# Performance work log

Measured on AMD Instinct MI355X. Metric: run time of the kernel, lower is better.

## Reference

```python
import jax, jax.numpy as jnp
import numpy as np

B, T, IN, H, FC, OUT = 512, 1024, 64, 128, 128, 1


def _glorot(key, shape, fan):
    bound = 1.0 / np.sqrt(fan)
    return jax.random.uniform(key, shape, jnp.float32, -bound, bound)


def setup_inputs() -> dict:
    key = jax.random.key(0)
    ks = jax.random.split(key, 16)
    inp = {"x": jax.random.normal(ks[0], (B, T, IN), jnp.float32)}
    # GRU layer 0 (input IN -> H), layer 1 (H -> H). PyTorch layout: [3H, in], [3H, H]
    inp["W_ih0"] = _glorot(ks[1], (3 * H, IN), H)
    inp["W_hh0"] = _glorot(ks[2], (3 * H, H), H)
    inp["b_ih0"] = _glorot(ks[3], (3 * H,), H)
    inp["b_hh0"] = _glorot(ks[4], (3 * H,), H)
    inp["W_ih1"] = _glorot(ks[5], (3 * H, H), H)
    inp["W_hh1"] = _glorot(ks[6], (3 * H, H), H)
    inp["b_ih1"] = _glorot(ks[7], (3 * H,), H)
    inp["b_hh1"] = _glorot(ks[8], (3 * H,), H)
    inp["fc1_w"] = _glorot(ks[9], (FC, H), H)
    inp["fc1_b"] = _glorot(ks[10], (FC,), H)
    inp["fc2_w"] = _glorot(ks[11], (OUT, FC), FC)
    inp["fc2_b"] = _glorot(ks[12], (OUT,), FC)
    return inp


def _gru_layer(x_seq, W_ih, W_hh, b_ih, b_hh):
    # x_seq: [T, B, in]. Precompute all input projections in one big GEMM.
    xg = jnp.einsum("tbi,gi->tbg", x_seq, W_ih) + b_ih  # [T, B, 3H]
    h0 = jnp.zeros((x_seq.shape[1], W_hh.shape[1]), x_seq.dtype)

    def step(h, xg_t):
        hg = h @ W_hh.T + b_hh  # [B, 3H]
        xr, xz, xn = jnp.split(xg_t, 3, axis=-1)
        hr, hz, hn = jnp.split(hg, 3, axis=-1)
        r = jax.nn.sigmoid(xr + hr)
        z = jax.nn.sigmoid(xz + hz)
        n = jnp.tanh(xn + r * hn)
        h_new = (1.0 - z) * n + z * h
        return h_new, h_new

    _, hs = jax.lax.scan(step, h0, xg)
    return hs  # [T, B, H]


def reference(x, W_ih0, W_hh0, b_ih0, b_hh0, W_ih1, W_hh1, b_ih1, b_hh1,
              fc1_w, fc1_b, fc2_w, fc2_b):
    xs = jnp.transpose(x, (1, 0, 2))  # [T, B, IN]
    h1 = _gru_layer(xs, W_ih0, W_hh0, b_ih0, b_hh0)  # dropout inactive (eval)
    h2 = _gru_layer(h1, W_ih1, W_hh1, b_ih1, b_hh1)
    last = h2[-1]  # [B, H] == gru_out[:, -1, :]
    y = jax.nn.relu(last @ fc1_w.T + fc1_b)
    return y @ fc2_w.T + fc2_b  # [B, OUT]
```

## Files before the change

### kernel.cpp

```cpp
#include <hip/hip_runtime.h>
#include <hip/hip_fp16.h>
#include <stdint.h>

#define TT   1024
#define NIN  64
#define HH   128
#define RPB  16
#define NWG  32
#define NTHR 512

#define FB_IH0 0
#define FB_HH0 48
#define FB_IH1 144
#define FB_HH1 240

typedef _Float16 f16x8 __attribute__((ext_vector_type(8)));
typedef float    f32x4 __attribute__((ext_vector_type(4)));
typedef _Float16 half2v __attribute__((ext_vector_type(2)));

__device__ __forceinline__ uint32_t pack2f(float a, float b) {
    half2v v; v[0] = (_Float16)a; v[1] = (_Float16)b;
    return __builtin_bit_cast(uint32_t, v);
}
__device__ __forceinline__ f16x8 bc8(uint4 u) { return __builtin_bit_cast(f16x8, u); }
__device__ __forceinline__ float sigm(float v)     { return 1.f / (1.f + __expf(-v)); }
__device__ __forceinline__ float tanhfast(float v) { return 2.f / (1.f + __expf(-2.f * v)) - 1.f; }

#define MF(c_, a_, b_) c_ = __builtin_amdgcn_mfma_f32_16x16x32_f16(bc8(a_), bc8(b_), c_, 0, 0, 0);

#define UNPK2(a_, b_, s_) { half2v t_ = __builtin_bit_cast(half2v, s_); a_ = (float)t_[0]; b_ = (float)t_[1]; }

#define CMB(ri_, CR_, CZ_, CX_, CH_, BR_, BZ_, BXX_, BHH_, HO_, NH_) { \
    float rg_ = sigm(CR_[ri_] + BR_);                                   \
    float zg_ = sigm(CZ_[ri_] + BZ_);                                   \
    float ng_ = tanhfast(CX_[ri_] + BXX_ + rg_ * (CH_[ri_] + BHH_));    \
    NH_ = ng_ + zg_ * (HO_ - ng_); HO_ = NH_; }

#define BARS() { asm volatile("s_waitcnt lgkmcnt(0)" ::: "memory");  \
                 __builtin_amdgcn_s_barrier();                        \
                 __builtin_amdgcn_sched_barrier(0);                   \
                 asm volatile("" ::: "memory"); }

__global__ __launch_bounds__(256) void pack_frags(
    const float* __restrict__ Wih0, const float* __restrict__ Whh0,
    const float* __restrict__ Wih1, const float* __restrict__ Whh1,
    uint4* __restrict__ ws)
{
    const int tid = blockIdx.x * 256 + threadIdx.x;
    const int f = tid >> 6, l = tid & 63;
    const float* W; int K, mt, kt;
    if (f < 48)       { W = Wih0; K = NIN; mt = f >> 1;        kt = f & 1; }
    else if (f < 144) { W = Whh0; K = HH;  mt = (f - 48) >> 2;  kt = (f - 48) & 3; }
    else if (f < 240) { W = Wih1; K = HH;  mt = (f - 144) >> 2; kt = (f - 144) & 3; }
    else              { W = Whh1; K = HH;  mt = (f - 240) >> 2; kt = (f - 240) & 3; }
    const float* s = W + (mt * 16 + (l & 15)) * K + kt * 32 + (l >> 4) * 8;
    uint4 o;
    o.x = pack2f(s[0], s[1]); o.y = pack2f(s[2], s[3]);
    o.z = pack2f(s[4], s[5]); o.w = pack2f(s[6], s[7]);
    ws[tid] = o;
}

__global__ __launch_bounds__(NTHR)
__attribute__((amdgpu_waves_per_eu(2, 2)))
void gru_mfma(
    const float* __restrict__ x, const uint4* __restrict__ wsA,
    const float* __restrict__ bih0, const float* __restrict__ bhh0,
    const float* __restrict__ bih1, const float* __restrict__ bhh1,
    const float* __restrict__ fc1w, const float* __restrict__ fc1b,
    const float* __restrict__ fc2w, const float* __restrict__ fc2b,
    float* __restrict__ out)
{
    __shared__ uint4 xF[2][2][64];
    __shared__ uint4 h0F[2][4][64];
    __shared__ uint4 h1F[2][4][64];
    __shared__ float h1f[RPB][HH];
    __shared__ float pFC[RPB][HH];
    __shared__ float p2[RPB][8];

    const int lid = threadIdx.x, w = lid >> 6, l = lid & 63;
    const int row0 = blockIdx.x * RPB;

#define DECLF(nm, idx) uint4 nm = wsA[(idx) * 64 + l];
    DECLF(a0r_i0, FB_IH0 + (w)*2 + 0)     DECLF(a0r_i1, FB_IH0 + (w)*2 + 1)
    DECLF(a0r_h0, FB_HH0 + (w)*4 + 0)     DECLF(a0r_h1, FB_HH0 + (w)*4 + 1)
    DECLF(a0r_h2, FB_HH0 + (w)*4 + 2)     DECLF(a0r_h3, FB_HH0 + (w)*4 + 3)
    DECLF(a0z_i0, FB_IH0 + (w+8)*2 + 0)   DECLF(a0z_i1, FB_IH0 + (w+8)*2 + 1)
    DECLF(a0z_h0, FB_HH0 + (w+8)*4 + 0)   DECLF(a0z_h1, FB_HH0 + (w+8)*4 + 1)
    DECLF(a0z_h2, FB_HH0 + (w+8)*4 + 2)   DECLF(a0z_h3, FB_HH0 + (w+8)*4 + 3)
    DECLF(a0n_i0, FB_IH0 + (16+w)*2 + 0)  DECLF(a0n_i1, FB_IH0 + (16+w)*2 + 1)
    DECLF(a0n_h0, FB_HH0 + (16+w)*4 + 0)  DECLF(a0n_h1, FB_HH0 + (16+w)*4 + 1)
    DECLF(a0n_h2, FB_HH0 + (16+w)*4 + 2)  DECLF(a0n_h3, FB_HH0 + (16+w)*4 + 3)
    DECLF(a1r_i0, FB_IH1 + (w)*4 + 0)     DECLF(a1r_i1, FB_IH1 + (w)*4 + 1)
    DECLF(a1r_i2, FB_IH1 + (w)*4 + 2)     DECLF(a1r_i3, FB_IH1 + (w)*4 + 3)
    DECLF(a1r_h0, FB_HH1 + (w)*4 + 0)     DECLF(a1r_h1, FB_HH1 + (w)*4 + 1)
    DECLF(a1r_h2, FB_HH1 + (w)*4 + 2)     DECLF(a1r_h3, FB_HH1 + (w)*4 + 3)
    DECLF(a1z_i0, FB_IH1 + (w+8)*4 + 0)   DECLF(a1z_i1, FB_IH1 + (w+8)*4 + 1)
    DECLF(a1z_i2, FB_IH1 + (w+8)*4 + 2)   DECLF(a1z_i3, FB_IH1 + (w+8)*4 + 3)
    DECLF(a1z_h0, FB_HH1 + (w+8)*4 + 0)   DECLF(a1z_h1, FB_HH1 + (w+8)*4 + 1)
    DECLF(a1z_h2, FB_HH1 + (w+8)*4 + 2)   DECLF(a1z_h3, FB_HH1 + (w+8)*4 + 3)
    DECLF(a1n_i0, FB_IH1 + (16+w)*4 + 0)  DECLF(a1n_i1, FB_IH1 + (16+w)*4 + 1)
    DECLF(a1n_i2, FB_IH1 + (16+w)*4 + 2)  DECLF(a1n_i3, FB_IH1 + (16+w)*4 + 3)
    DECLF(a1n_h0, FB_HH1 + (16+w)*4 + 0)  DECLF(a1n_h1, FB_HH1 + (16+w)*4 + 1)
    DECLF(a1n_h2, FB_HH1 + (16+w)*4 + 2)  DECLF(a1n_h3, FB_HH1 + (16+w)*4 + 3)

    const int j0 = 16 * w + 4 * (l >> 4);
    uint32_t B0r01 = pack2f(bih0[j0]+bhh0[j0],       bih0[j0+1]+bhh0[j0+1]);
    uint32_t B0r23 = pack2f(bih0[j0+2]+bhh0[j0+2],   bih0[j0+3]+bhh0[j0+3]);
    uint32_t B0z01 = pack2f(bih0[128+j0]+bhh0[128+j0],     bih0[129+j0]+bhh0[129+j0]);
    uint32_t B0z23 = pack2f(bih0[130+j0]+bhh0[130+j0],     bih0[131+j0]+bhh0[131+j0]);
    uint32_t B0x01 = pack2f(bih0[256+j0], bih0[257+j0]);
    uint32_t B0x23 = pack2f(bih0[258+j0], bih0[259+j0]);
    uint32_t B0h01 = pack2f(bhh0[256+j0], bhh0[257+j0]);
    uint32_t B0h23 = pack2f(bhh0[258+j0], bhh0[259+j0]);
    uint32_t B1r01 = pack2f(bih1[j0]+bhh1[j0],       bih1[j0+1]+bhh1[j0+1]);
    uint32_t B1r23 = pack2f(bih1[j0+2]+bhh1[j0+2],   bih1[j0+3]+bhh1[j0+3]);
    uint32_t B1z01 = pack2f(bih1[128+j0]+bhh1[128+j0],     bih1[129+j0]+bhh1[129+j0]);
    uint32_t B1z23 = pack2f(bih1[130+j0]+bhh1[130+j0],     bih1[131+j0]+bhh1[131+j0]);
    uint32_t B1x01 = pack2f(bih1[256+j0], bih1[257+j0]);
    uint32_t B1x23 = pack2f(bih1[258+j0], bih1[259+j0]);
    uint32_t B1h01 = pack2f(bhh1[256+j0], bhh1[257+j0]);
    uint32_t B1h23 = pack2f(bhh1[258+j0], bhh1[259+j0]);

    float h0o0 = 0.f, h0o1 = 0.f, h0o2 = 0.f, h0o3 = 0.f;
    float h1o0 = 0.f, h1o1 = 0.f, h1o2 = 0.f, h1o3 = 0.f;

    { uint4 z4 = {0u,0u,0u,0u};
      (&h0F[0][0][0])[lid] = z4;
      (&h1F[0][0][0])[lid] = z4; }

    const int xrow = lid >> 5, xk = (lid & 31) * 2;
    const float* xbase = x + (size_t)(row0 + xrow) * TT * NIN + xk;
    const int xoff = ((xk >> 5) << 10) + (((((xk & 31) >> 3) * 16) + xrow) << 4) + ((xk & 7) << 1);
    float2 xr2;
    { float2 v0 = *(const float2*)xbase;
      *(uint32_t*)((char*)&xF[0][0][0] + xoff) = pack2f(v0.x, v0.y);
      xr2 = *(const float2*)(xbase + NIN); }

    const int hoff = ((w >> 1) << 10)
                   + ((((2 * (w & 1) + ((l >> 4) >> 1)) * 16) + (l & 15)) << 4)
                   + (((l >> 4) & 1) << 3);

    __syncthreads();

    for (int i = 0; i <= TT; ++i) {
        const int p = i & 1;
        const uint4* bb0 = &h0F[p][0][0];
        uint4 bh00 = bb0[l], bh01 = bb0[64+l], bh02 = bb0[128+l], bh03 = bb0[192+l];

        if (i < TT) {
            const uint4* bxv = &xF[p][0][0];
            uint4 bx0 = bxv[l], bx1 = bxv[64 + l];
            f32x4 cr = {0,0,0,0}, cz = {0,0,0,0}, cx = {0,0,0,0}, ch = {0,0,0,0};
            MF(cr, a0r_i0, bx0)  MF(cr, a0r_i1, bx1)
            MF(cr, a0r_h0, bh00) MF(cr, a0r_h1, bh01) MF(cr, a0r_h2, bh02) MF(cr, a0r_h3, bh03)
            MF(cz, a0z_i0, bx0)  MF(cz, a0z_i1, bx1)
            MF(cz, a0z_h0, bh00) MF(cz, a0z_h1, bh01) MF(cz, a0z_h2, bh02) MF(cz, a0z_h3, bh03)
            MF(cx, a0n_i0, bx0)  MF(cx, a0n_i1, bx1)
            MF(ch, a0n_h0, bh00) MF(ch, a0n_h1, bh01) MF(ch, a0n_h2, bh02) MF(ch, a0n_h3, bh03)
            float vr0,vr1,vr2,vr3, vz0,vz1,vz2,vz3, vx0,vx1,vx2,vx3, vh0,vh1,vh2,vh3;
            UNPK2(vr0,vr1,B0r01) UNPK2(vr2,vr3,B0r23)
            UNPK2(vz0,vz1,B0z01) UNPK2(vz2,vz3,B0z23)
            UNPK2(vx0,vx1,B0x01) UNPK2(vx2,vx3,B0x23)
            UNPK2(vh0,vh1,B0h01) UNPK2(vh2,vh3,B0h23)
            float nh0, nh1, nh2, nh3;
            CMB(0, cr,cz,cx,ch, vr0,vz0,vx0,vh0, h0o0, nh0)
            CMB(1, cr,cz,cx,ch, vr1,vz1,vx1,vh1, h0o1, nh1)
            CMB(2, cr,cz,cx,ch, vr2,vz2,vx2,vh2, h0o2, nh2)
            CMB(3, cr,cz,cx,ch, vr3,vz3,vx3,vh3, h0o3, nh3)
            uint2 hw; hw.x = pack2f(nh0, nh1); hw.y = pack2f(nh2, nh3);
            *(uint2*)((char*)&h0F[1 - p][0][0] + hoff) = hw;
        }

        if (i >= 1) {
            const uint4* bb1 = &h1F[p][0][0];
            uint4 bh10 = bb1[l], bh11 = bb1[64+l], bh12 = bb1[128+l], bh13 = bb1[192+l];
            f32x4 cr = {0,0,0,0}, cz = {0,0,0,0}, cx = {0,0,0,0}, ch = {0,0,0,0};
            MF(cr, a1r_i0, bh00) MF(cr, a1r_i1, bh01) MF(cr, a1r_i2, bh02) MF(cr, a1r_i3, bh03)
            MF(cr, a1r_h0, bh10) MF(cr, a1r_h1, bh11) MF(cr, a1r_h2, bh12) MF(cr, a1r_h3, bh13)
            MF(cz, a1z_i0, bh00) MF(cz, a1z_i1, bh01) MF(cz, a1z_i2, bh02) MF(cz, a1z_i3, bh03)
            MF(cz, a1z_h0, bh10) MF(cz, a1z_h1, bh11) MF(cz, a1z_h2, bh12) MF(cz, a1z_h3, bh13)
            MF(cx, a1n_i0, bh00) MF(cx, a1n_i1, bh01) MF(cx, a1n_i2, bh02) MF(cx, a1n_i3, bh03)
            MF(ch, a1n_h0, bh10) MF(ch, a1n_h1, bh11) MF(ch, a1n_h2, bh12) MF(ch, a1n_h3, bh13)
            float vr0,vr1,vr2,vr3, vz0,vz1,vz2,vz3, vx0,vx1,vx2,vx3, vh0,vh1,vh2,vh3;
            UNPK2(vr0,vr1,B1r01) UNPK2(vr2,vr3,B1r23)
            UNPK2(vz0,vz1,B1z01) UNPK2(vz2,vz3,B1z23)
            UNPK2(vx0,vx1,B1x01) UNPK2(vx2,vx3,B1x23)
            UNPK2(vh0,vh1,B1h01) UNPK2(vh2,vh3,B1h23)
            float nh0, nh1, nh2, nh3;
            CMB(0, cr,cz,cx,ch, vr0,vz0,vx0,vh0, h1o0, nh0)
            CMB(1, cr,cz,cx,ch, vr1,vz1,vx1,vh1, h1o1, nh1)
            CMB(2, cr,cz,cx,ch, vr2,vz2,vx2,vh2, h1o2, nh2)
            CMB(3, cr,cz,cx,ch, vr3,vz3,vx3,vh3, h1o3, nh3)
            uint2 hw; hw.x = pack2f(nh0, nh1); hw.y = pack2f(nh2, nh3);
            *(uint2*)((char*)&h1F[1 - p][0][0] + hoff) = hw;
        }

        if (i + 1 < TT)
            *(uint32_t*)((char*)&xF[1 - p][0][0] + xoff) = pack2f(xr2.x, xr2.y);
        if (i + 2 < TT)
            xr2 = *(const float2*)(xbase + (size_t)(i + 2) * NIN);

        BARS();
    }

    { f32x4 hv; hv[0] = h1o0; hv[1] = h1o1; hv[2] = h1o2; hv[3] = h1o3;
      *(f32x4*)&h1f[l & 15][16 * w + 4 * (l >> 4)] = hv; }
    __syncthreads();

    { const int fcj = lid & 127, rb = lid >> 7;
      float a0 = fc1b[fcj], a1 = a0, a2 = a0, a3 = a0;
      const float* fw = fc1w + fcj * HH;
      #pragma unroll 4
      for (int k = 0; k < HH; ++k) {
          float wv = fw[k];
          a0 = fmaf(wv, h1f[rb][k], a0);
          a1 = fmaf(wv, h1f[rb + 4][k], a1);
          a2 = fmaf(wv, h1f[rb + 8][k], a2);
          a3 = fmaf(wv, h1f[rb + 12][k], a3);
      }
      float s2 = fc2w[fcj];
      pFC[rb][fcj]      = fmaxf(a0, 0.f) * s2;
      pFC[rb + 4][fcj]  = fmaxf(a1, 0.f) * s2;
      pFC[rb + 8][fcj]  = fmaxf(a2, 0.f) * s2;
      pFC[rb + 12][fcj] = fmaxf(a3, 0.f) * s2; }
    __syncthreads();
    if (lid < 128) {
        const int r = lid >> 3, seg = lid & 7;
        float s = 0.f;
        #pragma unroll
        for (int m2 = 0; m2 < 16; ++m2) s += pFC[r][seg * 16 + m2];
        p2[r][seg] = s;
    }
    __syncthreads();
    if (lid < RPB) {
        float s = fc2b[0];
        #pragma unroll
        for (int q = 0; q < 8; ++q) s += p2[lid][q];
        out[row0 + lid] = s;
    }
}

extern "C" void kernel_launch(void* const* d_in, const int* in_sizes, int n_in,
                              void* d_out, int out_size, void* d_ws, size_t ws_size,
                              hipStream_t stream) {
    const float* x    = (const float*)d_in[0];
    const float* Wih0 = (const float*)d_in[1];
    const float* Whh0 = (const float*)d_in[2];
    const float* bih0 = (const float*)d_in[3];
    const float* bhh0 = (const float*)d_in[4];
    const float* Wih1 = (const float*)d_in[5];
    const float* Whh1 = (const float*)d_in[6];
    const float* bih1 = (const float*)d_in[7];
    const float* bhh1 = (const float*)d_in[8];
    const float* fc1w = (const float*)d_in[9];
    const float* fc1b = (const float*)d_in[10];
    const float* fc2w = (const float*)d_in[11];
    const float* fc2b = (const float*)d_in[12];

    uint4* ws = (uint4*)d_ws;

    pack_frags<<<dim3(84), dim3(256), 0, stream>>>(Wih0, Whh0, Wih1, Whh1, ws);
    gru_mfma<<<dim3(NWG), dim3(NTHR), 0, stream>>>(
        x, ws, bih0, bhh0, bih1, bhh1, fc1w, fc1b, fc2w, fc2b, (float*)d_out);
}
```

Before: 2.228 ms.

## Fold biases into MFMA accumulator init and keep fp32 hidden state in LDS

```diff
diff --git a/kernel.cpp b/kernel.cpp
--- a/kernel.cpp
+++ b/kernel.cpp
@@ -30,11 +30,11 @@
 
 #define UNPK2(a_, b_, s_) { half2v t_ = __builtin_bit_cast(half2v, s_); a_ = (float)t_[0]; b_ = (float)t_[1]; }
 
-#define CMB(ri_, CR_, CZ_, CX_, CH_, BR_, BZ_, BXX_, BHH_, HO_, NH_) { \
-    float rg_ = sigm(CR_[ri_] + BR_);                                   \
-    float zg_ = sigm(CZ_[ri_] + BZ_);                                   \
-    float ng_ = tanhfast(CX_[ri_] + BXX_ + rg_ * (CH_[ri_] + BHH_));    \
-    NH_ = ng_ + zg_ * (HO_ - ng_); HO_ = NH_; }
+#define CMB2(ri_, HOv_, NH_) { \
+    float rg_ = sigm(cr[ri_]); \
+    float zg_ = sigm(cz[ri_]); \
+    float ng_ = tanhfast(fmaf(rg_, ch[ri_], cx[ri_])); \
+    NH_ = ng_ + zg_ * (HOv_[ri_] - ng_); }
 
 #define BARS() { asm volatile("s_waitcnt lgkmcnt(0)" ::: "memory");  \
                  __builtin_amdgcn_s_barrier();                        \
@@ -73,6 +73,7 @@
     __shared__ uint4 xF[2][2][64];
     __shared__ uint4 h0F[2][4][64];
     __shared__ uint4 h1F[2][4][64];
+    __shared__ f32x4 holdF[2][NTHR];
     __shared__ float h1f[RPB][HH];
     __shared__ float pFC[RPB][HH];
     __shared__ float p2[RPB][8];
@@ -121,12 +122,11 @@
     uint32_t B1h01 = pack2f(bhh1[256+j0], bhh1[257+j0]);
     uint32_t B1h23 = pack2f(bhh1[258+j0], bhh1[259+j0]);
 
-    float h0o0 = 0.f, h0o1 = 0.f, h0o2 = 0.f, h0o3 = 0.f;
-    float h1o0 = 0.f, h1o1 = 0.f, h1o2 = 0.f, h1o3 = 0.f;
-
     { uint4 z4 = {0u,0u,0u,0u};
       (&h0F[0][0][0])[lid] = z4;
-      (&h1F[0][0][0])[lid] = z4; }
+      (&h1F[0][0][0])[lid] = z4;
+      f32x4 zf = {0.f,0.f,0.f,0.f};
+      holdF[0][lid] = zf; holdF[1][lid] = zf; }
 
     const int xrow = lid >> 5, xk = (lid & 31) * 2;
     const float* xbase = x + (size_t)(row0 + xrow) * TT * NIN + xk;
@@ -146,51 +146,51 @@
         const int p = i & 1;
         const uint4* bb0 = &h0F[p][0][0];
         uint4 bh00 = bb0[l], bh01 = bb0[64+l], bh02 = bb0[128+l], bh03 = bb0[192+l];
+        const uint4* bb1 = &h1F[p][0][0];
+        uint4 bh10 = bb1[l], bh11 = bb1[64+l], bh12 = bb1[128+l], bh13 = bb1[192+l];
 
         if (i < TT) {
             const uint4* bxv = &xF[p][0][0];
             uint4 bx0 = bxv[l], bx1 = bxv[64 + l];
-            f32x4 cr = {0,0,0,0}, cz = {0,0,0,0}, cx = {0,0,0,0}, ch = {0,0,0,0};
+            float u0,u1,u2,u3;
+            UNPK2(u0,u1,B0r01) UNPK2(u2,u3,B0r23)  f32x4 cr = {u0,u1,u2,u3};
+            UNPK2(u0,u1,B0z01) UNPK2(u2,u3,B0z23)  f32x4 cz = {u0,u1,u2,u3};
+            UNPK2(u0,u1,B0x01) UNPK2(u2,u3,B0x23)  f32x4 cx = {u0,u1,u2,u3};
+            UNPK2(u0,u1,B0h01) UNPK2(u2,u3,B0h23)  f32x4 ch = {u0,u1,u2,u3};
             MF(cr, a0r_i0, bx0)  MF(cr, a0r_i1, bx1)
             MF(cr, a0r_h0, bh00) MF(cr, a0r_h1, bh01) MF(cr, a0r_h2, bh02) MF(cr, a0r_h3, bh03)
             MF(cz, a0z_i0, bx0)  MF(cz, a0z_i1, bx1)
             MF(cz, a0z_h0, bh00) MF(cz, a0z_h1, bh01) MF(cz, a0z_h2, bh02) MF(cz, a0z_h3, bh03)
             MF(cx, a0n_i0, bx0)  MF(cx, a0n_i1, bx1)
             MF(ch, a0n_h0, bh00) MF(ch, a0n_h1, bh01) MF(ch, a0n_h2, bh02) MF(ch, a0n_h3, bh03)
-            float vr0,vr1,vr2,vr3, vz0,vz1,vz2,vz3, vx0,vx1,vx2,vx3, vh0,vh1,vh2,vh3;
-            UNPK2(vr0,vr1,B0r01) UNPK2(vr2,vr3,B0r23)
-            UNPK2(vz0,vz1,B0z01) UNPK2(vz2,vz3,B0z23)
-            UNPK2(vx0,vx1,B0x01) UNPK2(vx2,vx3,B0x23)
-            UNPK2(vh0,vh1,B0h01) UNPK2(vh2,vh3,B0h23)
+            f32x4 hold = holdF[0][lid];
             float nh0, nh1, nh2, nh3;
-            CMB(0, cr,cz,cx,ch, vr0,vz0,vx0,vh0, h0o0, nh0)
-            CMB(1, cr,cz,cx,ch, vr1,vz1,vx1,vh1, h0o1, nh1)
-            CMB(2, cr,cz,cx,ch, vr2,vz2,vx2,vh2, h0o2, nh2)
-            CMB(3, cr,cz,cx,ch, vr3,vz3,vx3,vh3, h0o3, nh3)
+            CMB2(0, hold, nh0) CMB2(1, hold, nh1) CMB2(2, hold, nh2) CMB2(3, hold, nh3)
+            f32x4 hn_; hn_[0]=nh0; hn_[1]=nh1; hn_[2]=nh2; hn_[3]=nh3;
+            holdF[0][lid] = hn_;
             uint2 hw; hw.x = pack2f(nh0, nh1); hw.y = pack2f(nh2, nh3);
             *(uint2*)((char*)&h0F[1 - p][0][0] + hoff) = hw;
         }
 
+        __builtin_amdgcn_sched_barrier(0);
+
         if (i >= 1) {
-            const uint4* bb1 = &h1F[p][0][0];
-            uint4 bh10 = bb1[l], bh11 = bb1[64+l], bh12 = bb1[128+l], bh13 = bb1[192+l];
-            f32x4 cr = {0,0,0,0}, cz = {0,0,0,0}, cx = {0,0,0,0}, ch = {0,0,0,0};
+            float u0,u1,u2,u3;
+            UNPK2(u0,u1,B1r01) UNPK2(u2,u3,B1r23)  f32x4 cr = {u0,u1,u2,u3};
+            UNPK2(u0,u1,B1z01) UNPK2(u2,u3,B1z23)  f32x4 cz = {u0,u1,u2,u3};
+            UNPK2(u0,u1,B1x01) UNPK2(u2,u3,B1x23)  f32x4 cx = {u0,u1,u2,u3};
+            UNPK2(u0,u1,B1h01) UNPK2(u2,u3,B1h23)  f32x4 ch = {u0,u1,u2,u3};
             MF(cr, a1r_i0, bh00) MF(cr, a1r_i1, bh01) MF(cr, a1r_i2, bh02) MF(cr, a1r_i3, bh03)
             MF(cr, a1r_h0, bh10) MF(cr, a1r_h1, bh11) MF(cr, a1r_h2, bh12) MF(cr, a1r_h3, bh13)
             MF(cz, a1z_i0, bh00) MF(cz, a1z_i1, bh01) MF(cz, a1z_i2, bh02) MF(cz, a1z_i3, bh03)
             MF(cz, a1z_h0, bh10) MF(cz, a1z_h1, bh11) MF(cz, a1z_h2, bh12) MF(cz, a1z_h3, bh13)
             MF(cx, a1n_i0, bh00) MF(cx, a1n_i1, bh01) MF(cx, a1n_i2, bh02) MF(cx, a1n_i3, bh03)
             MF(ch, a1n_h0, bh10) MF(ch, a1n_h1, bh11) MF(ch, a1n_h2, bh12) MF(ch, a1n_h3, bh13)
-            float vr0,vr1,vr2,vr3, vz0,vz1,vz2,vz3, vx0,vx1,vx2,vx3, vh0,vh1,vh2,vh3;
-            UNPK2(vr0,vr1,B1r01) UNPK2(vr2,vr3,B1r23)
-            UNPK2(vz0,vz1,B1z01) UNPK2(vz2,vz3,B1z23)
-            UNPK2(vx0,vx1,B1x01) UNPK2(vx2,vx3,B1x23)
-            UNPK2(vh0,vh1,B1h01) UNPK2(vh2,vh3,B1h23)
+            f32x4 hold = holdF[1][lid];
             float nh0, nh1, nh2, nh3;
-            CMB(0, cr,cz,cx,ch, vr0,vz0,vx0,vh0, h1o0, nh0)
-            CMB(1, cr,cz,cx,ch, vr1,vz1,vx1,vh1, h1o1, nh1)
-            CMB(2, cr,cz,cx,ch, vr2,vz2,vx2,vh2, h1o2, nh2)
-            CMB(3, cr,cz,cx,ch, vr3,vz3,vx3,vh3, h1o3, nh3)
+            CMB2(0, hold, nh0) CMB2(1, hold, nh1) CMB2(2, hold, nh2) CMB2(3, hold, nh3)
+            f32x4 hn_; hn_[0]=nh0; hn_[1]=nh1; hn_[2]=nh2; hn_[3]=nh3;
+            holdF[1][lid] = hn_;
             uint2 hw; hw.x = pack2f(nh0, nh1); hw.y = pack2f(nh2, nh3);
             *(uint2*)((char*)&h1F[1 - p][0][0] + hoff) = hw;
         }
@@ -203,7 +203,7 @@
         BARS();
     }
 
-    { f32x4 hv; hv[0] = h1o0; hv[1] = h1o1; hv[2] = h1o2; hv[3] = h1o3;
+    { f32x4 hv = holdF[1][lid];
       *(f32x4*)&h1f[l & 15][16 * w + 4 * (l >> 4)] = hv; }
     __syncthreads();
 
```

After: 2.423 ms. +8.7%, slower.
